# Optimization experiments

Hardware: AMD Instinct MI355X
Metric: run time of the kernel (lower is better)

## Reference

```python
import jax, jax.numpy as jnp
import numpy as np

DIM = 768
HEADS = 12

def setup_inputs() -> dict:
    key = jax.random.key(0)
    ks = jax.random.split(key, 5)
    x = jax.random.normal(ks[0], (8, 1024, DIM), dtype=jnp.float32)
    s = 1.0 / np.sqrt(DIM)
    W_qkv = jax.random.normal(ks[1], (DIM, 3 * DIM), dtype=jnp.float32) * s
    b_qkv = jax.random.normal(ks[2], (3 * DIM,), dtype=jnp.float32) * 0.01
    W_proj = jax.random.normal(ks[3], (DIM, DIM), dtype=jnp.float32) * s
    b_proj = jax.random.normal(ks[4], (DIM,), dtype=jnp.float32) * 0.01
    return {"x": x, "W_qkv": W_qkv, "b_qkv": b_qkv, "W_proj": W_proj, "b_proj": b_proj}

def reference(x, W_qkv, b_qkv, W_proj, b_proj):
    B, T, D = x.shape
    H = HEADS
    hd = D // H
    scale = hd ** -0.5
    qkv = x @ W_qkv + b_qkv                      # [B,T,3D]
    qkv = qkv.reshape(B, T, 3, H, hd)
    q, k, v = jnp.moveaxis(qkv, 2, 0)            # each [B,T,H,hd]
    q = jnp.transpose(q, (0, 2, 1, 3))           # [B,H,T,hd]
    k = jnp.transpose(k, (0, 2, 1, 3))
    v = jnp.transpose(v, (0, 2, 1, 3))
    attn = jnp.einsum('bhqd,bhkd->bhqk', q, k) * scale
    attn = jax.nn.softmax(attn, axis=-1)
    y = jnp.einsum('bhqk,bhkd->bhqd', attn, v)   # [B,H,T,hd]
    y = jnp.transpose(y, (0, 2, 1, 3)).reshape(B, T, D)
    return y @ W_proj + b_proj
```

## Files before the change

### kernel.cpp

```cpp
#include <hip/hip_runtime.h>

typedef unsigned short u16;
typedef __attribute__((ext_vector_type(8))) short short8;
typedef __attribute__((ext_vector_type(4))) short short4v;
typedef __attribute__((ext_vector_type(2))) int int2v;
typedef __attribute__((ext_vector_type(4))) float f32x4;

#define DIM   768
#define HEADS 12
#define HD    64
#define BATCH 8
#define SEQ   1024
#define MTOK  (BATCH*SEQ)
#define NQKV  (3*DIM)
#define KPAD  72
#define EPAD  66
#define PSZ   ((size_t)BATCH*HEADS*SEQ*HD)
#define SCQ   0.1803368801f

__device__ __forceinline__ u16 f2bf(float f) {
  unsigned x = __float_as_uint(f);
  x += 0x7fffu + ((x >> 16) & 1u);
  return (u16)(x >> 16);
}

__device__ __forceinline__ void gload16(const u16* g, u16* l) {
  __builtin_amdgcn_global_load_lds(
      (const __attribute__((address_space(1))) unsigned int*)g,
      (__attribute__((address_space(3))) unsigned int*)l, 16, 0, 0);
}

#define XBLK 6144
#define QTBLK 1728
__global__ void cvt_all_k(const float* __restrict__ x,
                          const float* __restrict__ Wqkv,
                          const float* __restrict__ Wproj,
                          u16* __restrict__ xb, u16* __restrict__ wqkvt,
                          u16* __restrict__ wprojt) {
  __shared__ u16 tile[32][33];
  const int blk = blockIdx.x;
  if (blk < XBLK) {
    const int i = blk * 256 + threadIdx.x;
    float4 f = ((const float4*)x)[i];
    short4v o;
    o.x = (short)f2bf(f.x); o.y = (short)f2bf(f.y);
    o.z = (short)f2bf(f.z); o.w = (short)f2bf(f.w);
    ((short4v*)xb)[i] = o;
    return;
  }
  const float* in; u16* out; int K, N, n0, k0;
  if (blk < XBLK + QTBLK) {
    const int t = blk - XBLK;
    in = Wqkv; out = wqkvt; K = DIM; N = NQKV;
    n0 = (t % (NQKV / 32)) * 32; k0 = (t / (NQKV / 32)) * 32;
  } else {
    const int t = blk - XBLK - QTBLK;
    in = Wproj; out = wprojt; K = DIM; N = DIM;
    n0 = (t % (DIM / 32)) * 32; k0 = (t / (DIM / 32)) * 32;
  }
  const int tx = threadIdx.x & 31, ty = threadIdx.x >> 5;
  #pragma unroll
  for (int i = 0; i < 32; i += 8)
    tile[ty + i][tx] = f2bf(in[(size_t)(k0 + ty + i) * N + n0 + tx]);
  __syncthreads();
  #pragma unroll
  for (int i = 0; i < 32; i += 8)
    out[(size_t)(n0 + ty + i) * K + k0 + tx] = tile[tx][ty + i];
}

__global__ __launch_bounds__(256)
void gemm_qkv(const u16* __restrict__ A, const u16* __restrict__ Bt,
              const float* __restrict__ bias, u16* __restrict__ qkv) {
  __shared__ __align__(16) u16 smem[4 * 128 * 32];
  u16* lA0 = smem;
  u16* lA1 = smem + 128 * 32;
  u16* lB0 = smem + 2 * 128 * 32;
  u16* lB1 = smem + 3 * 128 * 32;
  const int w = threadIdx.x >> 6, lane = threadIdx.x & 63;
  const int l15 = lane & 15, quad = lane >> 4;
  const int b_ = blockIdx.x;
  const int xcd = b_ & 7, j = b_ >> 3;
  const int m0 = ((j & 7) * 8 + xcd) * 128;
  const int n0 = (j >> 3) * 128;
  const int wm = (w >> 1) * 64, wn = (w & 1) * 64;

  f32x4 acc[4][4] = {};

  const int ar = threadIdx.x >> 2, ak = (threadIdx.x & 3) * 8;
  const u16* ga = A  + (size_t)(m0 + ar) * DIM + ak;
  const u16* gb = Bt + (size_t)(n0 + ar) * DIM + ak;
  const int lo = threadIdx.x * 8;

  for (int k0 = 0; k0 < DIM; k0 += 64) {
    #pragma unroll
    for (int t = 0; t < 2; ++t) {
      gload16(ga + (size_t)t * 64 * DIM + k0,      lA0 + lo + t * 2048);
      gload16(ga + (size_t)t * 64 * DIM + k0 + 32, lA1 + lo + t * 2048);
      gload16(gb + (size_t)t * 64 * DIM + k0,      lB0 + lo + t * 2048);
      gload16(gb + (size_t)t * 64 * DIM + k0 + 32, lB1 + lo + t * 2048);
    }
    __syncthreads();

    #pragma unroll
    for (int kh = 0; kh < 2; ++kh) {
      const u16* lAh = kh ? lA1 : lA0;
      const u16* lBh = kh ? lB1 : lB0;
      short8 af[4], bfr[4];
      #pragma unroll
      for (int mt = 0; mt < 4; ++mt)
        af[mt] = *(const short8*)&lAh[(wm + mt * 16 + l15) * 32 + quad * 8];
      #pragma unroll
      for (int nt = 0; nt < 4; ++nt)
        bfr[nt] = *(const short8*)&lBh[(wn + nt * 16 + l15) * 32 + quad * 8];
      #pragma unroll
      for (int mt = 0; mt < 4; ++mt)
        #pragma unroll
        for (int nt = 0; nt < 4; ++nt)
          acc[mt][nt] = __builtin_amdgcn_mfma_f32_16x16x32_bf16(af[mt], bfr[nt], acc[mt][nt], 0, 0, 0);
    }
    __syncthreads();
  }

  const int bb = m0 >> 10;
  const int tb0 = (m0 & 1023) + wm;
  const int nh = n0 + wn;
  const int part = nh / DIM, idx = nh - part * DIM;
  const int h = idx >> 6;

  float bnl[4];
  #pragma unroll
  for (int nt = 0; nt < 4; ++nt) bnl[nt] = bias[nh + nt * 16 + l15];

  if (part < 2) {
    u16* dstbase = qkv + part * PSZ + ((size_t)(bb * HEADS + h) * SEQ + tb0) * HD;
    const float qsc = (part == 0) ? SCQ : 1.0f;
    const int erow = lane >> 3, ec8 = (lane & 7) * 8;
    #pragma unroll
    for (int mt = 0; mt < 4; ++mt) {
      u16* ep = smem + w * (16 * EPAD) + (mt & 1) * (4 * 16 * EPAD);
      #pragma unroll
      for (int nt = 0; nt < 4; ++nt)
        #pragma unroll
        for (int r = 0; r < 4; ++r)
          ep[(quad * 4 + r) * EPAD + nt * 16 + l15] = f2bf((acc[mt][nt][r] + bnl[nt]) * qsc);
      #pragma unroll
      for (int j2 = 0; j2 < 2; ++j2) {
        const int trow = j2 * 8 + erow;
        short8 vrow = *(const short8*)&ep[trow * EPAD + ec8];
        *(short8*)(dstbase + (size_t)(mt * 16 + trow) * HD + ec8) = vrow;
      }
    }
  } else {
    u16* vrow0 = qkv + 2 * PSZ + (size_t)(bb * HEADS + h) * HD * SEQ;
    #pragma unroll
    for (int nt = 0; nt < 4; ++nt) {
      const int d = nt * 16 + l15;
      u16* trow = vrow0 + (size_t)d * SEQ + tb0 + quad * 4;
      #pragma unroll
      for (int mt = 0; mt < 4; ++mt) {
        short4v pv;
        pv.x = (short)f2bf(acc[mt][nt][0] + bnl[nt]);
        pv.y = (short)f2bf(acc[mt][nt][1] + bnl[nt]);
        pv.z = (short)f2bf(acc[mt][nt][2] + bnl[nt]);
        pv.w = (short)f2bf(acc[mt][nt][3] + bnl[nt]);
        *(short4v*)(trow + mt * 16) = pv;
      }
    }
  }
}

__global__ __launch_bounds__(256)
void gemm_proj(const u16* __restrict__ A, const u16* __restrict__ Bt,
               const float* __restrict__ bias, float* __restrict__ outF) {
  __shared__ __align__(16) u16 smem[2 * 128 * 32 + 2 * 64 * 32];
  u16* lA0 = smem;
  u16* lA1 = smem + 128 * 32;
  u16* lB0 = smem + 2 * 128 * 32;
  u16* lB1 = lB0 + 64 * 32;
  const int w = threadIdx.x >> 6, lane = threadIdx.x & 63;
  const int l15 = lane & 15, quad = lane >> 4;
  const int b_ = blockIdx.x;
  const int xcd = b_ & 7, j = b_ >> 3;
  const int m0 = ((j & 7) * 8 + xcd) * 128;
  const int n0 = (j >> 3) * 64;
  const int wm = w * 32;

  f32x4 acc[2][4] = {};

  const int ar = threadIdx.x >> 2, ak = (threadIdx.x & 3) * 8;
  const u16* ga = A  + (size_t)(m0 + ar) * DIM + ak;
  const u16* gb = Bt + (size_t)(n0 + ar) * DIM + ak;
  const int lo = threadIdx.x * 8;

  for (int k0 = 0; k0 < DIM; k0 += 64) {
    #pragma unroll
    for (int t = 0; t < 2; ++t) {
      gload16(ga + (size_t)t * 64 * DIM + k0,      lA0 + lo + t * 2048);
      gload16(ga + (size_t)t * 64 * DIM + k0 + 32, lA1 + lo + t * 2048);
    }
    gload16(gb + k0,      lB0 + lo);
    gload16(gb + k0 + 32, lB1 + lo);
    __syncthreads();

    #pragma unroll
    for (int kh = 0; kh < 2; ++kh) {
      const u16* lAh = kh ? lA1 : lA0;
      const u16* lBh = kh ? lB1 : lB0;
      short8 af[2], bfr[4];
      #pragma unroll
      for (int mt = 0; mt < 2; ++mt)
        af[mt] = *(const short8*)&lAh[(wm + mt * 16 + l15) * 32 + quad * 8];
      #pragma unroll
      for (int nt = 0; nt < 4; ++nt)
        bfr[nt] = *(const short8*)&lBh[(nt * 16 + l15) * 32 + quad * 8];
      #pragma unroll
      for (int mt = 0; mt < 2; ++mt)
        #pragma unroll
        for (int nt = 0; nt < 4; ++nt)
          acc[mt][nt] = __builtin_amdgcn_mfma_f32_16x16x32_bf16(af[mt], bfr[nt], acc[mt][nt], 0, 0, 0);
    }
    __syncthreads();
  }

  #pragma unroll
  for (int nt = 0; nt < 4; ++nt) {
    const int n = n0 + nt * 16 + l15;
    const float bn = bias[n];
    #pragma unroll
    for (int mt = 0; mt < 2; ++mt)
      #pragma unroll
      for (int r = 0; r < 4; ++r) {
        const int m = m0 + wm + mt * 16 + quad * 4 + r;
        outF[(size_t)m * DIM + n] = acc[mt][nt][r] + bn;
      }
  }
}

__global__ __launch_bounds__(256)
void attn_k(const u16* __restrict__ qb, const u16* __restrict__ kb,
            const u16* __restrict__ vtb, u16* __restrict__ yb) {
  const int bh = blockIdx.x, qt = blockIdx.y;
  const int w = threadIdx.x >> 6, lane = threadIdx.x & 63;
  const int l15 = lane & 15, quad = lane >> 4;

  __shared__ __align__(16) u16 lK[64 * KPAD];
  __shared__ __align__(16) u16 lV[64 * KPAD];
  __shared__ __align__(16) u16 lP[4][32 * KPAD];

  const u16* qb0 = qb + ((size_t)bh * SEQ + qt * 128 + w * 32 + l15) * HD;
  short8 aq[2][2];
  #pragma unroll
  for (int qg = 0; qg < 2; ++qg) {
    aq[qg][0] = *(const short8*)(qb0 + (size_t)qg * 16 * HD + quad * 8);
    aq[qg][1] = *(const short8*)(qb0 + (size_t)qg * 16 * HD + 32 + quad * 8);
  }

  f32x4 o[2][4] = {};
  float rs[2] = {0.f, 0.f};

  const u16* kcbase = kb + (size_t)bh * SEQ * HD;
  const u16* vbase  = vtb + (size_t)bh * HD * SEQ;
  u16* lPw = &lP[w][0];

  const int cid0 = threadIdx.x, cid1 = threadIdx.x + 256;
  const int sofs0 = (cid0 >> 3) * KPAD + (cid0 & 7) * 8;
  const int sofs1 = (cid1 >> 3) * KPAD + (cid1 & 7) * 8;
  const u16* vg0 = vbase + (size_t)(cid0 >> 3) * SEQ + (cid0 & 7) * 8;
  const u16* vg1 = vbase + (size_t)(cid1 >> 3) * SEQ + (cid1 & 7) * 8;

  short8 pk0 = *(const short8*)(kcbase + cid0 * 8);
  short8 pk1 = *(const short8*)(kcbase + cid1 * 8);
  short8 pv0 = *(const short8*)vg0;
  short8 pv1 = *(const short8*)vg1;

  for (int kc = 0; kc < 16; ++kc) {
    *(short8*)&lK[sofs0] = pk0;
    *(short8*)&lK[sofs1] = pk1;
    *(short8*)&lV[sofs0] = pv0;
    *(short8*)&lV[sofs1] = pv1;
    __syncthreads();

    const int kn = (kc < 15) ? kc + 1 : 15;
    pk0 = *(const short8*)(kcbase + kn * 64 * HD + cid0 * 8);
    pk1 = *(const short8*)(kcbase + kn * 64 * HD + cid1 * 8);
    pv0 = *(const short8*)(vg0 + kn * 64);
    pv1 = *(const short8*)(vg1 + kn * 64);

    short8 ak0[4], ak1[4], bv0[4], bv1[4];
    #pragma unroll
    for (int nt = 0; nt < 4; ++nt) {
      ak0[nt] = *(const short8*)&lK[(nt * 16 + l15) * KPAD + quad * 8];
      ak1[nt] = *(const short8*)&lK[(nt * 16 + l15) * KPAD + 32 + quad * 8];
      bv0[nt] = *(const short8*)&lV[(nt * 16 + l15) * KPAD + quad * 8];
      bv1[nt] = *(const short8*)&lV[(nt * 16 + l15) * KPAD + 32 + quad * 8];
    }

    #pragma unroll
    for (int qg = 0; qg < 2; ++qg) {
      f32x4 st[4] = {};
      #pragma unroll
      for (int nt = 0; nt < 4; ++nt) {
        st[nt] = __builtin_amdgcn_mfma_f32_16x16x32_bf16(ak0[nt], aq[qg][0], st[nt], 0, 0, 0);
        st[nt] = __builtin_amdgcn_mfma_f32_16x16x32_bf16(ak1[nt], aq[qg][1], st[nt], 0, 0, 0);
      }

      #pragma unroll
      for (int nt = 0; nt < 4; ++nt) {
        float p0 = __builtin_amdgcn_exp2f(st[nt][0]);
        float p1 = __builtin_amdgcn_exp2f(st[nt][1]);
        float p2 = __builtin_amdgcn_exp2f(st[nt][2]);
        float p3 = __builtin_amdgcn_exp2f(st[nt][3]);
        float t0 = __uint_as_float(__float_as_uint(p0) & 0xffff0000u);
        float t1 = __uint_as_float(__float_as_uint(p1) & 0xffff0000u);
        float t2 = __uint_as_float(__float_as_uint(p2) & 0xffff0000u);
        float t3 = __uint_as_float(__float_as_uint(p3) & 0xffff0000u);
        rs[qg] += (t0 + t1) + (t2 + t3);
        int2v pk;
        pk.x = (int)__builtin_amdgcn_perm(__float_as_uint(p1), __float_as_uint(p0), 0x07060302u);
        pk.y = (int)__builtin_amdgcn_perm(__float_as_uint(p3), __float_as_uint(p2), 0x07060302u);
        *(int2v*)&lPw[(qg * 16 + l15) * KPAD + nt * 16 + quad * 4] = pk;
      }
      const short8 ap0 = *(const short8*)&lPw[(qg * 16 + l15) * KPAD + quad * 8];
      const short8 ap1 = *(const short8*)&lPw[(qg * 16 + l15) * KPAD + 32 + quad * 8];
      #pragma unroll
      for (int nt = 0; nt < 4; ++nt) {
        o[qg][nt] = __builtin_amdgcn_mfma_f32_16x16x32_bf16(ap0, bv0[nt], o[qg][nt], 0, 0, 0);
        o[qg][nt] = __builtin_amdgcn_mfma_f32_16x16x32_bf16(ap1, bv1[nt], o[qg][nt], 0, 0, 0);
      }
    }
    __syncthreads();
  }

  const int b = bh / HEADS, h = bh % HEADS;
  #pragma unroll
  for (int qg = 0; qg < 2; ++qg) {
    rs[qg] += __shfl_xor(rs[qg], 16);
    rs[qg] += __shfl_xor(rs[qg], 32);
    #pragma unroll
    for (int r = 0; r < 4; ++r) {
      const float inv = 1.0f / __shfl(rs[qg], quad * 4 + r, 16);
      #pragma unroll
      for (int nt = 0; nt < 4; ++nt)
        lPw[(qg * 16 + quad * 4 + r) * KPAD + nt * 16 + l15] = f2bf(o[qg][nt][r] * inv);
    }
  }

  u16* dst = yb + ((size_t)b * SEQ + qt * 128 + w * 32) * DIM + h * HD;
  const int erow = lane >> 3, ec8 = (lane & 7) * 8;
  #pragma unroll
  for (int j = 0; j < 4; ++j) {
    const int trow = j * 8 + erow;
    short8 vrow = *(const short8*)&lPw[trow * KPAD + ec8];
    *(short8*)(dst + (size_t)trow * DIM + ec8) = vrow;
  }
}

extern "C" void kernel_launch(void* const* d_in, const int* in_sizes, int n_in,
                              void* d_out, int out_size, void* d_ws, size_t ws_size,
                              hipStream_t stream) {
  const float* x     = (const float*)d_in[0];
  const float* Wqkv  = (const float*)d_in[1];
  const float* bqkv  = (const float*)d_in[2];
  const float* Wproj = (const float*)d_in[3];
  const float* bproj = (const float*)d_in[4];
  float* out = (float*)d_out;

  u16* xb     = (u16*)d_ws;
  u16* wqkvt  = xb + (size_t)MTOK * DIM;
  u16* wprojt = wqkvt + (size_t)NQKV * DIM;
  u16* qkv_b  = wprojt + (size_t)DIM * DIM;
  u16* y_b    = qkv_b + 3 * PSZ;

  cvt_all_k<<<XBLK + QTBLK + (DIM / 32) * (DIM / 32), 256, 0, stream>>>(
      x, Wqkv, Wproj, xb, wqkvt, wprojt);

  gemm_qkv<<<1152, 256, 0, stream>>>(xb, wqkvt, bqkv, qkv_b);

  attn_k<<<dim3(BATCH * HEADS, SEQ / 128), 256, 0, stream>>>(
      qkv_b, qkv_b + PSZ, qkv_b + 2 * PSZ, y_b);

  gemm_proj<<<768, 256, 0, stream>>>(y_b, wprojt, bproj, out);
}
```

Measured before the change: 193.4 us.

## Double-buffer GEMM LDS tiles and load attention K/V straight from global

Both projection GEMMs now use two LDS stages, so the next K-slice is loaded while MFMAs run on the current one, with one barrier per iteration instead of two. The attention kernel drops its shared K/V staging and block barriers. Each wave instead reads its K and V^T fragments directly from global memory and relies on cache reuse across the four waves. This trades barrier stalls and LDS copies for more LDS in the GEMMs (lower occupancy) and for repeated global/L2 traffic and exposed load latency in attention.

```diff
diff --git a/kernel.cpp b/kernel.cpp
--- a/kernel.cpp
+++ b/kernel.cpp
@@ -71,11 +71,7 @@
 __global__ __launch_bounds__(256)
 void gemm_qkv(const u16* __restrict__ A, const u16* __restrict__ Bt,
               const float* __restrict__ bias, u16* __restrict__ qkv) {
-  __shared__ __align__(16) u16 smem[4 * 128 * 32];
-  u16* lA0 = smem;
-  u16* lA1 = smem + 128 * 32;
-  u16* lB0 = smem + 2 * 128 * 32;
-  u16* lB1 = smem + 3 * 128 * 32;
+  __shared__ __align__(16) u16 smem[8 * 128 * 32];
   const int w = threadIdx.x >> 6, lane = threadIdx.x & 63;
   const int l15 = lane & 15, quad = lane >> 4;
   const int b_ = blockIdx.x;
@@ -91,20 +87,29 @@
   const u16* gb = Bt + (size_t)(n0 + ar) * DIM + ak;
   const int lo = threadIdx.x * 8;
 
-  for (int k0 = 0; k0 < DIM; k0 += 64) {
+  auto qstage = [&](int c, int k0) {
+    u16* base = smem + c * 16384;
     #pragma unroll
     for (int t = 0; t < 2; ++t) {
-      gload16(ga + (size_t)t * 64 * DIM + k0,      lA0 + lo + t * 2048);
-      gload16(ga + (size_t)t * 64 * DIM + k0 + 32, lA1 + lo + t * 2048);
-      gload16(gb + (size_t)t * 64 * DIM + k0,      lB0 + lo + t * 2048);
-      gload16(gb + (size_t)t * 64 * DIM + k0 + 32, lB1 + lo + t * 2048);
-    }
-    __syncthreads();
-
+      gload16(ga + (size_t)t * 64 * DIM + k0,      base + lo + t * 2048);
+      gload16(ga + (size_t)t * 64 * DIM + k0 + 32, base + 4096  + lo + t * 2048);
+      gload16(gb + (size_t)t * 64 * DIM + k0,      base + 8192  + lo + t * 2048);
+      gload16(gb + (size_t)t * 64 * DIM + k0 + 32, base + 12288 + lo + t * 2048);
+    }
+  };
+
+  qstage(0, 0);
+  __syncthreads();
+
+  #pragma unroll
+  for (int it = 0; it < 12; ++it) {
+    const int cur = it & 1;
+    if (it < 11) qstage(cur ^ 1, (it + 1) * 64);
+    const u16* hb = smem + cur * 16384;
     #pragma unroll
     for (int kh = 0; kh < 2; ++kh) {
-      const u16* lAh = kh ? lA1 : lA0;
-      const u16* lBh = kh ? lB1 : lB0;
+      const u16* lAh = hb + kh * 4096;
+      const u16* lBh = hb + 8192 + kh * 4096;
       short8 af[4], bfr[4];
       #pragma unroll
       for (int mt = 0; mt < 4; ++mt)
@@ -172,11 +177,7 @@
 __global__ __launch_bounds__(256)
 void gemm_proj(const u16* __restrict__ A, const u16* __restrict__ Bt,
                const float* __restrict__ bias, float* __restrict__ outF) {
-  __shared__ __align__(16) u16 smem[2 * 128 * 32 + 2 * 64 * 32];
-  u16* lA0 = smem;
-  u16* lA1 = smem + 128 * 32;
-  u16* lB0 = smem + 2 * 128 * 32;
-  u16* lB1 = lB0 + 64 * 32;
+  __shared__ __align__(16) u16 smem[2 * 12288];
   const int w = threadIdx.x >> 6, lane = threadIdx.x & 63;
   const int l15 = lane & 15, quad = lane >> 4;
   const int b_ = blockIdx.x;
@@ -192,20 +193,29 @@
   const u16* gb = Bt + (size_t)(n0 + ar) * DIM + ak;
   const int lo = threadIdx.x * 8;
 
-  for (int k0 = 0; k0 < DIM; k0 += 64) {
+  auto pstage = [&](int c, int k0) {
+    u16* base = smem + c * 12288;
     #pragma unroll
     for (int t = 0; t < 2; ++t) {
-      gload16(ga + (size_t)t * 64 * DIM + k0,      lA0 + lo + t * 2048);
-      gload16(ga + (size_t)t * 64 * DIM + k0 + 32, lA1 + lo + t * 2048);
-    }
-    gload16(gb + k0,      lB0 + lo);
-    gload16(gb + k0 + 32, lB1 + lo);
-    __syncthreads();
-
+      gload16(ga + (size_t)t * 64 * DIM + k0,      base + lo + t * 2048);
+      gload16(ga + (size_t)t * 64 * DIM + k0 + 32, base + 4096 + lo + t * 2048);
+    }
+    gload16(gb + k0,      base + 8192  + lo);
+    gload16(gb + k0 + 32, base + 10240 + lo);
+  };
+
+  pstage(0, 0);
+  __syncthreads();
+
+  #pragma unroll
+  for (int it = 0; it < 12; ++it) {
+    const int cur = it & 1;
+    if (it < 11) pstage(cur ^ 1, (it + 1) * 64);
+    const u16* hb = smem + cur * 12288;
     #pragma unroll
     for (int kh = 0; kh < 2; ++kh) {
-      const u16* lAh = kh ? lA1 : lA0;
-      const u16* lBh = kh ? lB1 : lB0;
+      const u16* lAh = hb + kh * 4096;
+      const u16* lBh = hb + 8192 + kh * 2048;
       short8 af[2], bfr[4];
       #pragma unroll
       for (int mt = 0; mt < 2; ++mt)
@@ -243,8 +253,6 @@
   const int w = threadIdx.x >> 6, lane = threadIdx.x & 63;
   const int l15 = lane & 15, quad = lane >> 4;
 
-  __shared__ __align__(16) u16 lK[64 * KPAD];
-  __shared__ __align__(16) u16 lV[64 * KPAD];
   __shared__ __align__(16) u16 lP[4][32 * KPAD];
 
   const u16* qb0 = qb + ((size_t)bh * SEQ + qt * 128 + w * 32 + l15) * HD;
@@ -262,37 +270,17 @@
   const u16* vbase  = vtb + (size_t)bh * HD * SEQ;
   u16* lPw = &lP[w][0];
 
-  const int cid0 = threadIdx.x, cid1 = threadIdx.x + 256;
-  const int sofs0 = (cid0 >> 3) * KPAD + (cid0 & 7) * 8;
-  const int sofs1 = (cid1 >> 3) * KPAD + (cid1 & 7) * 8;
-  const u16* vg0 = vbase + (size_t)(cid0 >> 3) * SEQ + (cid0 & 7) * 8;
-  const u16* vg1 = vbase + (size_t)(cid1 >> 3) * SEQ + (cid1 & 7) * 8;
-
-  short8 pk0 = *(const short8*)(kcbase + cid0 * 8);
-  short8 pk1 = *(const short8*)(kcbase + cid1 * 8);
-  short8 pv0 = *(const short8*)vg0;
-  short8 pv1 = *(const short8*)vg1;
-
   for (int kc = 0; kc < 16; ++kc) {
-    *(short8*)&lK[sofs0] = pk0;
-    *(short8*)&lK[sofs1] = pk1;
-    *(short8*)&lV[sofs0] = pv0;
-    *(short8*)&lV[sofs1] = pv1;
-    __syncthreads();
-
-    const int kn = (kc < 15) ? kc + 1 : 15;
-    pk0 = *(const short8*)(kcbase + kn * 64 * HD + cid0 * 8);
-    pk1 = *(const short8*)(kcbase + kn * 64 * HD + cid1 * 8);
-    pv0 = *(const short8*)(vg0 + kn * 64);
-    pv1 = *(const short8*)(vg1 + kn * 64);
+    const u16* kk = kcbase + (size_t)kc * 64 * HD;
+    const u16* vv = vbase + kc * 64;
 
     short8 ak0[4], ak1[4], bv0[4], bv1[4];
     #pragma unroll
     for (int nt = 0; nt < 4; ++nt) {
-      ak0[nt] = *(const short8*)&lK[(nt * 16 + l15) * KPAD + quad * 8];
-      ak1[nt] = *(const short8*)&lK[(nt * 16 + l15) * KPAD + 32 + quad * 8];
-      bv0[nt] = *(const short8*)&lV[(nt * 16 + l15) * KPAD + quad * 8];
-      bv1[nt] = *(const short8*)&lV[(nt * 16 + l15) * KPAD + 32 + quad * 8];
+      ak0[nt] = *(const short8*)(kk + (size_t)(nt * 16 + l15) * HD + quad * 8);
+      ak1[nt] = *(const short8*)(kk + (size_t)(nt * 16 + l15) * HD + 32 + quad * 8);
+      bv0[nt] = *(const short8*)(vv + (size_t)(nt * 16 + l15) * SEQ + quad * 8);
+      bv1[nt] = *(const short8*)(vv + (size_t)(nt * 16 + l15) * SEQ + 32 + quad * 8);
     }
 
     #pragma unroll
@@ -328,7 +316,6 @@
         o[qg][nt] = __builtin_amdgcn_mfma_f32_16x16x32_bf16(ap1, bv1[nt], o[qg][nt], 0, 0, 0);
       }
     }
-    __syncthreads();
   }
 
   const int b = bh / HEADS, h = bh % HEADS;
```

New measurement: 232.5 us. +20.2%, slower.
